# Kernel tuning notes

Measured on AMD Instinct MI355X. Metric: run time of the kernel, lower is better.

The kernel has to match this reference:

```python
import jax, jax.numpy as jnp
import numpy as np

EMBED_DIM = 768
NUM_HEADS = 12
MLP_SCALE = 4


def setup_inputs() -> dict:
    key = jax.random.key(0)
    ks = jax.random.split(key, 12)
    D = EMBED_DIM
    H = D * MLP_SCALE
    s = lambda fan_in: 1.0 / np.sqrt(fan_in)
    inp = {
        "x": jax.random.normal(ks[0], (16, 1024, D), dtype=jnp.float32),
        # shared LayerNorm params
        "ln_g": jnp.ones((D,), jnp.float32),
        "ln_b": jnp.zeros((D,), jnp.float32),
        # fused QKV projection: Linear(D, 3D)
        "w_qkv": jax.random.uniform(ks[1], (3 * D, D), jnp.float32, -s(D), s(D)),
        "b_qkv": jax.random.uniform(ks[2], (3 * D,), jnp.float32, -s(D), s(D)),
        "w_out": jax.random.uniform(ks[3], (D, D), jnp.float32, -s(D), s(D)),
        "b_out": jax.random.uniform(ks[4], (D,), jnp.float32, -s(D), s(D)),
        # MLP: Linear(D, 4D) -> GELU -> Linear(4D, D); dropout=0 at eval
        "w_fc1": jax.random.uniform(ks[5], (H, D), jnp.float32, -s(D), s(D)),
        "b_fc1": jax.random.uniform(ks[6], (H,), jnp.float32, -s(D), s(D)),
        "w_fc2": jax.random.uniform(ks[7], (D, H), jnp.float32, -s(H), s(H)),
        "b_fc2": jax.random.uniform(ks[8], (D,), jnp.float32, -s(H), s(H)),
    }
    return inp


def _layernorm(x, g, b, eps=1e-5):
    mu = jnp.mean(x, axis=-1, keepdims=True)
    var = jnp.var(x, axis=-1, keepdims=True)
    return (x - mu) * jax.lax.rsqrt(var + eps) * g + b


def _mha(x, w_qkv, b_qkv, w_out, b_out):
    B, S, D = x.shape
    hd = D // NUM_HEADS
    qkv = x @ w_qkv.T + b_qkv                      # [B,S,3D]
    qkv = qkv.reshape(B, S, 3, NUM_HEADS, hd)
    q, k, v = qkv[:, :, 0], qkv[:, :, 1], qkv[:, :, 2]  # [B,S,H,hd]
    # NOTE: original scales by 1/sqrt(embed_dim), not 1/sqrt(head_dim)
    scores = jnp.einsum("bqhd,bkhd->bhqk", q, k) / jnp.sqrt(jnp.float32(D))
    attn = jax.nn.softmax(scores, axis=-1)
    out = jnp.einsum("bhqk,bkhd->bqhd", attn, v).reshape(B, S, D)
    return out @ w_out.T + b_out


def reference(x, ln_g, ln_b, w_qkv, b_qkv, w_out, b_out, w_fc1, b_fc1, w_fc2, b_fc2):
    # x = x + MHA(LN(x)); shared LayerNorm params for both uses
    x = x + _mha(_layernorm(x, ln_g, ln_b), w_qkv, b_qkv, w_out, b_out)
    h = _layernorm(x, ln_g, ln_b)
    h = jax.nn.gelu(h @ w_fc1.T + b_fc1, approximate=False)
    x = x + (h @ w_fc2.T + b_fc2)
    return x
```

## Files before the change

### kernel.cpp

```cpp
#include <hip/hip_runtime.h>
#include <math.h>

#define DIM    768
#define NB     16
#define SEQ    1024
#define NTOK   (NB*SEQ)
#define HEADS  12
#define HD     64
#define HMLP   3072
#define QKVN   2304

typedef _Float16 f16x8 __attribute__((ext_vector_type(8)));
typedef _Float16 f16x4 __attribute__((ext_vector_type(4)));
typedef float    f32x4 __attribute__((ext_vector_type(4)));

typedef __attribute__((address_space(3))) unsigned int       lds_u32;
typedef __attribute__((address_space(1))) const unsigned int glb_u32;

__device__ __forceinline__ void gload16(const _Float16* g, _Float16* l) {
    __builtin_amdgcn_global_load_lds((glb_u32*)g, (lds_u32*)l, 16, 0, 0);
}

__global__ __launch_bounds__(256) void ln_kernel(const float* __restrict__ x,
                                                 const float* __restrict__ g,
                                                 const float* __restrict__ b,
                                                 _Float16* __restrict__ out) {
    const int t = blockIdx.x;
    const float* xp = x + (size_t)t * DIM;
    float v[3];
    float s = 0.f, ss = 0.f;
#pragma unroll
    for (int u = 0; u < 3; ++u) {
        v[u] = xp[threadIdx.x + 256 * u];
        s += v[u];
        ss += v[u] * v[u];
    }
#pragma unroll
    for (int m = 1; m < 64; m <<= 1) {
        s  += __shfl_xor(s, m);
        ss += __shfl_xor(ss, m);
    }
    __shared__ float rs[4], rss[4];
    const int wave = threadIdx.x >> 6;
    if ((threadIdx.x & 63) == 0) { rs[wave] = s; rss[wave] = ss; }
    __syncthreads();
    s  = rs[0] + rs[1] + rs[2] + rs[3];
    ss = rss[0] + rss[1] + rss[2] + rss[3];
    const float mu  = s * (1.0f / DIM);
    const float var = ss * (1.0f / DIM) - mu * mu;
    const float rst = 1.0f / sqrtf(var + 1e-5f);
    _Float16* op = out + (size_t)t * DIM;
#pragma unroll
    for (int u = 0; u < 3; ++u) {
        const int c = threadIdx.x + 256 * u;
        op[c] = (_Float16)((v[u] - mu) * rst * g[c] + b[c]);
    }
}

__global__ __launch_bounds__(256) void cast_kernel(const float* __restrict__ in,
                                                   _Float16* __restrict__ out, int n) {
    const int i = (blockIdx.x * 256 + threadIdx.x) * 4;
    if (i < n) {
        const float4 v = *(const float4*)(in + i);
        f16x4 o;
        o[0] = (_Float16)v.x; o[1] = (_Float16)v.y;
        o[2] = (_Float16)v.z; o[3] = (_Float16)v.w;
        *(f16x4*)(out + i) = o;
    }
}

template <int EPI, typename OUT_T>
__global__ __launch_bounds__(256) void gemm_f16(const _Float16* __restrict__ A,
                                                const _Float16* __restrict__ Bw,
                                                const float* __restrict__ bias,
                                                const float* __restrict__ res,
                                                OUT_T* __restrict__ C,
                                                int M, int N, int K) {
    __shared__ _Float16 As[2][128 * 32];
    __shared__ _Float16 Bs[2][128 * 32];

    const int tid  = threadIdx.x;
    const int lane = tid & 63;
    const int wave = tid >> 6;
    const int wr = wave >> 1;
    const int wc = wave & 1;
    const int n0 = blockIdx.x * 128;
    const int m0 = blockIdx.y * 128;

    const int sr = tid >> 2;
    const int sp = tid & 3;

    f32x4 acc[4][4] = {};

    auto stage = [&](int buf, int k0) {
#pragma unroll
        for (int h = 0; h < 2; ++h) {
            const int r  = sr + h * 64;
            const int kc = sp ^ ((r >> 1) & 3);
            const size_t goff = (size_t)r * K + k0 + kc * 8;
            gload16(A  + (size_t)m0 * K + goff, &As[buf][tid * 8 + h * 2048]);
            gload16(Bw + (size_t)n0 * K + goff, &Bs[buf][tid * 8 + h * 2048]);
        }
    };

    auto compute = [&](int buf) {
        f16x8 a[4], b[4];
#pragma unroll
        for (int m = 0; m < 4; ++m) {
            const int row = wr * 64 + m * 16 + (lane & 15);
            const int p   = (lane >> 4) ^ ((row >> 1) & 3);
            a[m] = *(const f16x8*)&As[buf][row * 32 + p * 8];
        }
#pragma unroll
        for (int n = 0; n < 4; ++n) {
            const int row = wc * 64 + n * 16 + (lane & 15);
            const int p   = (lane >> 4) ^ ((row >> 1) & 3);
            b[n] = *(const f16x8*)&Bs[buf][row * 32 + p * 8];
        }
#pragma unroll
        for (int m = 0; m < 4; ++m)
#pragma unroll
            for (int n = 0; n < 4; ++n)
                acc[m][n] = __builtin_amdgcn_mfma_f32_16x16x32_f16(a[m], b[n], acc[m][n], 0, 0, 0);
    };

    const int NT = K / 32;
    stage(0, 0);
    __syncthreads();
    int cur = 0;
    for (int t = 0; t < NT; ++t) {
        if (t + 1 < NT) stage(cur ^ 1, (t + 1) * 32);
        compute(cur);
        __syncthreads();
        cur ^= 1;
    }

    const int col0 = n0 + wc * 64 + (lane & 15);
#pragma unroll
    for (int m = 0; m < 4; ++m) {
#pragma unroll
        for (int j = 0; j < 4; ++j) {
            const size_t row = (size_t)(m0 + wr * 64 + m * 16 + (lane >> 4) * 4 + j);
#pragma unroll
            for (int n = 0; n < 4; ++n) {
                const int col = col0 + n * 16;
                float c = acc[m][n][j] + bias[col];
                if (EPI == 2) c = 0.5f * c * (1.0f + erff(c * 0.70710678118f));
                if (EPI == 1) c += res[row * N + col];
                C[row * N + col] = (OUT_T)c;
            }
        }
    }
}

__global__ __launch_bounds__(256) void attn_kernel(const _Float16* __restrict__ qkv,
                                                   _Float16* __restrict__ out) {
    __shared__ _Float16 K_lds[64 * 72];
    __shared__ _Float16 Vt[64 * 72];
    __shared__ _Float16 P_lds[4][16 * 72];

    const int q0 = blockIdx.x * 64;
    const int h  = blockIdx.y;
    const int b  = blockIdx.z;
    const float SCALE2 = 0.05205879570f;

    const int tid  = threadIdx.x;
    const int lane = tid & 63;
    const int w    = tid >> 6;
    const int g    = lane >> 4;
    const int c    = lane & 15;

    const int skey = tid >> 3;
    const int sdc  = tid & 7;

    const size_t base = (size_t)b * SEQ * QKVN + (size_t)h * HD;

    f16x8 aq[2];
#pragma unroll
    for (int kk = 0; kk < 2; ++kk)
        aq[kk] = *(const f16x8*)(qkv + base + (size_t)(q0 + w * 16 + c) * QKVN + kk * 32 + g * 8);

    f32x4 o[4] = {};
    float mrow[4] = {-1e30f, -1e30f, -1e30f, -1e30f};
    float lrow[4] = {};

    for (int kt = 0; kt < 16; ++kt) {
        const int k0 = kt * 64;
        __syncthreads();
#pragma unroll
        for (int it = 0; it < 2; ++it) {
            const int key = skey + it * 32;
            const f16x8 kv = *(const f16x8*)(qkv + base + 768  + (size_t)(k0 + key) * QKVN + sdc * 8);
            const f16x8 vv = *(const f16x8*)(qkv + base + 1536 + (size_t)(k0 + key) * QKVN + sdc * 8);
            *(f16x8*)&K_lds[key * 72 + sdc * 8] = kv;
            const int pc = (key >> 3) ^ sdc;
#pragma unroll
            for (int e = 0; e < 8; ++e)
                Vt[(sdc * 8 + e) * 72 + pc * 8 + (key & 7)] = vv[e];
        }
        __syncthreads();

        f32x4 s[4] = {};
#pragma unroll
        for (int n = 0; n < 4; ++n) {
#pragma unroll
            for (int kk = 0; kk < 2; ++kk) {
                const f16x8 bk = *(const f16x8*)&K_lds[(n * 16 + c) * 72 + (kk * 4 + g) * 8];
                s[n] = __builtin_amdgcn_mfma_f32_16x16x32_f16(aq[kk], bk, s[n], 0, 0, 0);
            }
        }

        float p[4][4];
#pragma unroll
        for (int j = 0; j < 4; ++j) {
            float sv[4];
#pragma unroll
            for (int n = 0; n < 4; ++n) sv[n] = s[n][j] * SCALE2;
            float mx = fmaxf(fmaxf(sv[0], sv[1]), fmaxf(sv[2], sv[3]));
#pragma unroll
            for (int m = 1; m < 16; m <<= 1) mx = fmaxf(mx, __shfl_xor(mx, m));
            const float mnew  = fmaxf(mrow[j], mx);
            const float alpha = exp2f(mrow[j] - mnew);
            float rsum = 0.f;
#pragma unroll
            for (int n = 0; n < 4; ++n) {
                p[n][j] = exp2f(sv[n] - mnew);
                rsum += p[n][j];
            }
#pragma unroll
            for (int m = 1; m < 16; m <<= 1) rsum += __shfl_xor(rsum, m);
            lrow[j] = lrow[j] * alpha + rsum;
            mrow[j] = mnew;
#pragma unroll
            for (int n = 0; n < 4; ++n) o[n][j] *= alpha;
        }

#pragma unroll
        for (int j = 0; j < 4; ++j)
#pragma unroll
            for (int n = 0; n < 4; ++n)
                P_lds[w][(g * 4 + j) * 72 + n * 16 + c] = (_Float16)p[n][j];

#pragma unroll
        for (int kk = 0; kk < 2; ++kk) {
            const f16x8 ap = *(const f16x8*)&P_lds[w][c * 72 + kk * 32 + g * 8];
#pragma unroll
            for (int n = 0; n < 4; ++n) {
                const int dp = n * 16 + c;
                const int pc = (kk * 4 + g) ^ (dp >> 3);
                const f16x8 bv = *(const f16x8*)&Vt[dp * 72 + pc * 8];
                o[n] = __builtin_amdgcn_mfma_f32_16x16x32_f16(ap, bv, o[n], 0, 0, 0);
            }
        }
    }

#pragma unroll
    for (int j = 0; j < 4; ++j) {
        const size_t row = (size_t)(b * SEQ + q0 + w * 16 + g * 4 + j);
        const float inv = 1.0f / lrow[j];
#pragma unroll
        for (int n = 0; n < 4; ++n)
            out[row * DIM + h * HD + n * 16 + c] = (_Float16)(o[n][j] * inv);
    }
}

extern "C" void kernel_launch(void* const* d_in, const int* in_sizes, int n_in,
                              void* d_out, int out_size, void* d_ws, size_t ws_size,
                              hipStream_t stream) {
    const float* x     = (const float*)d_in[0];
    const float* ln_g  = (const float*)d_in[1];
    const float* ln_b  = (const float*)d_in[2];
    const float* w_qkv = (const float*)d_in[3];
    const float* b_qkv = (const float*)d_in[4];
    const float* w_out = (const float*)d_in[5];
    const float* b_out = (const float*)d_in[6];
    const float* w_fc1 = (const float*)d_in[7];
    const float* b_fc1 = (const float*)d_in[8];
    const float* w_fc2 = (const float*)d_in[9];
    const float* b_fc2 = (const float*)d_in[10];
    float* out = (float*)d_out;

    char* ws = (char*)d_ws;
    _Float16* wq16   = (_Float16*)(ws);
    _Float16* wo16   = (_Float16*)(ws + 3538944);
    _Float16* wf1_16 = (_Float16*)(ws + 4718592);
    _Float16* wf2_16 = (_Float16*)(ws + 9437184);
    _Float16* ln16   = (_Float16*)(ws + 14155776);
    _Float16* qkv16  = (_Float16*)(ws + 39321600);
    _Float16* attn16 = (_Float16*)(ws + 114819072);
    _Float16* h16    = qkv16;

    cast_kernel<<<(QKVN * DIM) / 1024, 256, 0, stream>>>(w_qkv, wq16, QKVN * DIM);
    cast_kernel<<<(DIM * DIM) / 1024, 256, 0, stream>>>(w_out, wo16, DIM * DIM);
    cast_kernel<<<(HMLP * DIM) / 1024, 256, 0, stream>>>(w_fc1, wf1_16, HMLP * DIM);
    cast_kernel<<<(DIM * HMLP) / 1024, 256, 0, stream>>>(w_fc2, wf2_16, DIM * HMLP);

    ln_kernel<<<NTOK, 256, 0, stream>>>(x, ln_g, ln_b, ln16);
    gemm_f16<0, _Float16><<<dim3(QKVN / 128, NTOK / 128), 256, 0, stream>>>(
        ln16, wq16, b_qkv, nullptr, qkv16, NTOK, QKVN, DIM);
    attn_kernel<<<dim3(SEQ / 64, HEADS, NB), 256, 0, stream>>>(qkv16, attn16);
    gemm_f16<1, float><<<dim3(DIM / 128, NTOK / 128), 256, 0, stream>>>(
        attn16, wo16, b_out, x, out, NTOK, DIM, DIM);
    ln_kernel<<<NTOK, 256, 0, stream>>>(out, ln_g, ln_b, ln16);
    gemm_f16<2, _Float16><<<dim3(HMLP / 128, NTOK / 128), 256, 0, stream>>>(
        ln16, wf1_16, b_fc1, nullptr, h16, NTOK, HMLP, DIM);
    gemm_f16<1, float><<<dim3(DIM / 128, NTOK / 128), 256, 0, stream>>>(
        h16, wf2_16, b_fc2, out, out, NTOK, DIM, HMLP);
}
```

Before: 739.5 us.

## Compute transposed S=K·Q in attention to keep P in registers and skip LDS

The attention kernel now computes the transposed score tile (K as the A operand, Q as B), so each lane holds one query row's scores. The softmax row reductions then shrink to two cross-group shuffles, and P can be packed straight into MFMA A-operands without a round trip through LDS. K tiles are loaded with direct global-to-LDS loads into an XOR-swizzled unpadded layout, and the MFMA sections are wrapped in s_setprio. This removes the P_lds buffer and its stores and loads, at the cost of extra shuffles to redistribute alpha and l to the output layout and split 8-byte V reads.

```diff
diff --git a/kernel.cpp b/kernel.cpp
--- a/kernel.cpp
+++ b/kernel.cpp
@@ -155,9 +155,8 @@
 
 __global__ __launch_bounds__(256) void attn_kernel(const _Float16* __restrict__ qkv,
                                                    _Float16* __restrict__ out) {
-    __shared__ _Float16 K_lds[64 * 72];
+    __shared__ _Float16 K_lds[64 * 64];
     __shared__ _Float16 Vt[64 * 72];
-    __shared__ _Float16 P_lds[4][16 * 72];
 
     const int q0 = blockIdx.x * 64;
     const int h  = blockIdx.y;
@@ -172,6 +171,8 @@
 
     const int skey = tid >> 3;
     const int sdc  = tid & 7;
+    const int kkey = tid >> 3;
+    const int kchunk = (tid & 7) ^ ((tid >> 3) & 7);
 
     const size_t base = (size_t)b * SEQ * QKVN + (size_t)h * HD;
 
@@ -181,86 +182,101 @@
         aq[kk] = *(const f16x8*)(qkv + base + (size_t)(q0 + w * 16 + c) * QKVN + kk * 32 + g * 8);
 
     f32x4 o[4] = {};
-    float mrow[4] = {-1e30f, -1e30f, -1e30f, -1e30f};
-    float lrow[4] = {};
+    float mrow = -1e30f, lrow = 0.f;
 
     for (int kt = 0; kt < 16; ++kt) {
         const int k0 = kt * 64;
         __syncthreads();
 #pragma unroll
         for (int it = 0; it < 2; ++it) {
-            const int key = skey + it * 32;
-            const f16x8 kv = *(const f16x8*)(qkv + base + 768  + (size_t)(k0 + key) * QKVN + sdc * 8);
-            const f16x8 vv = *(const f16x8*)(qkv + base + 1536 + (size_t)(k0 + key) * QKVN + sdc * 8);
-            *(f16x8*)&K_lds[key * 72 + sdc * 8] = kv;
-            const int pc = (key >> 3) ^ sdc;
+            const int key = kkey + it * 32;
+            gload16(qkv + base + 768 + (size_t)(k0 + key) * QKVN + kchunk * 8,
+                    &K_lds[it * 2048 + tid * 8]);
+            const int vkey = skey + it * 32;
+            const f16x8 vv = *(const f16x8*)(qkv + base + 1536 + (size_t)(k0 + vkey) * QKVN + sdc * 8);
+            const int pc = (vkey >> 3) ^ sdc;
 #pragma unroll
             for (int e = 0; e < 8; ++e)
-                Vt[(sdc * 8 + e) * 72 + pc * 8 + (key & 7)] = vv[e];
+                Vt[(sdc * 8 + e) * 72 + pc * 8 + (vkey & 7)] = vv[e];
         }
         __syncthreads();
 
         f32x4 s[4] = {};
-#pragma unroll
-        for (int n = 0; n < 4; ++n) {
+        __builtin_amdgcn_s_setprio(1);
+#pragma unroll
+        for (int kb = 0; kb < 4; ++kb) {
 #pragma unroll
             for (int kk = 0; kk < 2; ++kk) {
-                const f16x8 bk = *(const f16x8*)&K_lds[(n * 16 + c) * 72 + (kk * 4 + g) * 8];
-                s[n] = __builtin_amdgcn_mfma_f32_16x16x32_f16(aq[kk], bk, s[n], 0, 0, 0);
-            }
-        }
+                const f16x8 ak = *(const f16x8*)&K_lds[(kb * 16 + c) * 64 + (((kk * 4 + g) ^ (c & 7)) * 8)];
+                s[kb] = __builtin_amdgcn_mfma_f32_16x16x32_f16(ak, aq[kk], s[kb], 0, 0, 0);
+            }
+        }
+        __builtin_amdgcn_s_setprio(0);
 
         float p[4][4];
+        float mx = -1e30f;
+#pragma unroll
+        for (int kb = 0; kb < 4; ++kb)
+#pragma unroll
+            for (int j = 0; j < 4; ++j) {
+                p[kb][j] = s[kb][j] * SCALE2;
+                mx = fmaxf(mx, p[kb][j]);
+            }
+        mx = fmaxf(mx, __shfl_xor(mx, 16));
+        mx = fmaxf(mx, __shfl_xor(mx, 32));
+        const float mnew  = fmaxf(mrow, mx);
+        const float alpha = exp2f(mrow - mnew);
+        float rsum = 0.f;
+#pragma unroll
+        for (int kb = 0; kb < 4; ++kb)
+#pragma unroll
+            for (int j = 0; j < 4; ++j) {
+                p[kb][j] = exp2f(p[kb][j] - mnew);
+                rsum += p[kb][j];
+            }
+        rsum += __shfl_xor(rsum, 16);
+        rsum += __shfl_xor(rsum, 32);
+        lrow = lrow * alpha + rsum;
+        mrow = mnew;
+
 #pragma unroll
         for (int j = 0; j < 4; ++j) {
-            float sv[4];
-#pragma unroll
-            for (int n = 0; n < 4; ++n) sv[n] = s[n][j] * SCALE2;
-            float mx = fmaxf(fmaxf(sv[0], sv[1]), fmaxf(sv[2], sv[3]));
-#pragma unroll
-            for (int m = 1; m < 16; m <<= 1) mx = fmaxf(mx, __shfl_xor(mx, m));
-            const float mnew  = fmaxf(mrow[j], mx);
-            const float alpha = exp2f(mrow[j] - mnew);
-            float rsum = 0.f;
+            const float aj = __shfl(alpha, g * 4 + j);
+#pragma unroll
+            for (int n = 0; n < 4; ++n) o[n][j] *= aj;
+        }
+
+        f16x8 pa[2];
+#pragma unroll
+        for (int kk = 0; kk < 2; ++kk)
+#pragma unroll
+            for (int e = 0; e < 8; ++e)
+                pa[kk][e] = (_Float16)p[2 * kk + (e >> 2)][e & 3];
+
+        __builtin_amdgcn_s_setprio(1);
+#pragma unroll
+        for (int kk = 0; kk < 2; ++kk) {
 #pragma unroll
             for (int n = 0; n < 4; ++n) {
-                p[n][j] = exp2f(sv[n] - mnew);
-                rsum += p[n][j];
-            }
-#pragma unroll
-            for (int m = 1; m < 16; m <<= 1) rsum += __shfl_xor(rsum, m);
-            lrow[j] = lrow[j] * alpha + rsum;
-            mrow[j] = mnew;
-#pragma unroll
-            for (int n = 0; n < 4; ++n) o[n][j] *= alpha;
-        }
-
-#pragma unroll
-        for (int j = 0; j < 4; ++j)
-#pragma unroll
-            for (int n = 0; n < 4; ++n)
-                P_lds[w][(g * 4 + j) * 72 + n * 16 + c] = (_Float16)p[n][j];
-
-#pragma unroll
-        for (int kk = 0; kk < 2; ++kk) {
-            const f16x8 ap = *(const f16x8*)&P_lds[w][c * 72 + kk * 32 + g * 8];
-#pragma unroll
-            for (int n = 0; n < 4; ++n) {
-                const int dp = n * 16 + c;
-                const int pc = (kk * 4 + g) ^ (dp >> 3);
-                const f16x8 bv = *(const f16x8*)&Vt[dp * 72 + pc * 8];
-                o[n] = __builtin_amdgcn_mfma_f32_16x16x32_f16(ap, bv, o[n], 0, 0, 0);
-            }
-        }
+                const int d = n * 16 + c;
+                const int ch0 = (4 * kk + (g >> 1)) ^ (d >> 3);
+                const int ch1 = (4 * kk + 2 + (g >> 1)) ^ (d >> 3);
+                union { uint2 r[2]; f16x8 v; } bb;
+                bb.r[0] = *(const uint2*)&Vt[d * 72 + ch0 * 8 + (g & 1) * 4];
+                bb.r[1] = *(const uint2*)&Vt[d * 72 + ch1 * 8 + (g & 1) * 4];
+                o[n] = __builtin_amdgcn_mfma_f32_16x16x32_f16(pa[kk], bb.v, o[n], 0, 0, 0);
+            }
+        }
+        __builtin_amdgcn_s_setprio(0);
     }
 
 #pragma unroll
     for (int j = 0; j < 4; ++j) {
+        const float linv = 1.0f / __shfl(lrow, g * 4 + j);
         const size_t row = (size_t)(b * SEQ + q0 + w * 16 + g * 4 + j);
-        const float inv = 1.0f / lrow[j];
 #pragma unroll
         for (int n = 0; n < 4; ++n)
-            out[row * DIM + h * HD + n * 16 + c] = (_Float16)(o[n][j] * inv);
+            out[row * DIM + h * HD + n * 16 + c] = (_Float16)(o[n][j] * linv);
     }
 }
 
```

Result: faster. 705.4 us (-4.6%).
